# Kernel tuning notes

Measured on AMD Instinct MI355X. Metric: run time of the kernel, lower is better.

Reference implementation:

```python
import jax, jax.numpy as jnp
import numpy as np

DIM = 192
HEADS = 4
EPS = 1e-12  # F.normalize default eps


def setup_inputs() -> dict:
    key = jax.random.key(0)
    ks = jax.random.split(key, 5)
    b, c, h, w = 8, DIM, 128, 128
    x = jax.random.normal(ks[0], (b, c, h, w), dtype=jnp.float32)
    w_qkv = jax.random.normal(ks[1], (3 * DIM, DIM, 1, 1), dtype=jnp.float32) * (1.0 / np.sqrt(DIM))
    w_dw = jax.random.normal(ks[2], (3 * DIM, 1, 3, 3), dtype=jnp.float32) * (1.0 / 3.0)
    w_proj = jax.random.normal(ks[3], (DIM, DIM, 1, 1), dtype=jnp.float32) * (1.0 / np.sqrt(DIM))
    temperature = jnp.ones((HEADS, 1, 1), dtype=jnp.float32)
    return {"x": x, "w_qkv": w_qkv, "w_dw": w_dw, "w_proj": w_proj, "temperature": temperature}


def _conv1x1(x, w):
    # x: [b,c,h,w], w: [o,c,1,1] -> [b,o,h,w]
    return jnp.einsum('bchw,oc->bohw', x, w[:, :, 0, 0])


def _dwconv3x3(x, w):
    # depthwise 3x3, padding=1; x: [b,C,h,w], w: [C,1,3,3]
    C = x.shape[1]
    return jax.lax.conv_general_dilated(
        x, w, window_strides=(1, 1), padding=((1, 1), (1, 1)),
        dimension_numbers=('NCHW', 'OIHW', 'NCHW'), feature_group_count=C)


def _l2norm(x):
    n = jnp.linalg.norm(x, axis=-1, keepdims=True)
    return x / jnp.maximum(n, EPS)


def reference(x, w_qkv, w_dw, w_proj, temperature):
    b, c, h, w = x.shape
    head = HEADS
    ch = c // head  # channels per head
    qkv = _dwconv3x3(_conv1x1(x, w_qkv), w_dw)  # [b, 3c, h, w]
    q, k, v = jnp.split(qkv, 3, axis=1)  # each [b, c, h, w]

    def to_heads(t):
        # b (head ch) h w -> b head h (ch w)
        t = t.reshape(b, head, ch, h, w)
        return t.transpose(0, 1, 3, 2, 4).reshape(b, head, h, ch * w)

    q1 = _l2norm(to_heads(q))
    k1 = _l2norm(to_heads(k))
    v1 = to_heads(v)
    # attn over height dim: [b, head, h, h]
    attn = jax.nn.softmax(jnp.einsum('bhif,bhjf->bhij', q1, k1) * temperature[None], axis=-1)
    out = jnp.einsum('bhij,bhjf->bhif', attn, v1)  # [b, head, h, ch*w]
    # b head h (ch w) -> b (head ch) h w
    out = out.reshape(b, head, h, ch, w).transpose(0, 1, 3, 2, 4).reshape(b, c, h, w)
    return _conv1x1(out, w_proj)
```

## Files before the change

kernel.cpp:

```cpp
#include <hip/hip_runtime.h>
#include <hip/hip_bf16.h>

#define BB 8
#define CC 192
#define C3 576
#define NH 4
#define CH 48
#define HH 128
#define WW 128
#define HW 16384
#define FF 6144

typedef short s16x8 __attribute__((ext_vector_type(8)));
typedef float f32x4 __attribute__((ext_vector_type(4)));

constexpr size_t SPM = 32ull * 128 * 128;

constexpr size_t OFF_XT  = 0;
constexpr size_t SZ_XT   = (size_t)BB * HW * CC * 2;
constexpr size_t OFF_WQ  = OFF_XT + SZ_XT;
constexpr size_t SZ_WQ   = (size_t)C3 * CC * 2;
constexpr size_t OFF_WP  = OFF_WQ + SZ_WQ;
constexpr size_t SZ_WP   = (size_t)CC * CC * 2;
constexpr size_t OFF_RAW = OFF_WP + SZ_WP;
constexpr size_t SZ_RAW  = (size_t)BB * C3 * HW * 2;
constexpr size_t OFF_DW  = OFF_RAW + SZ_RAW;
constexpr size_t OFF_SP  = OFF_DW + SZ_RAW;
constexpr size_t OFF_ATB = OFF_SP + 8 * SPM * 4;
constexpr size_t OFF_RQ  = OFF_ATB + 32ull * 128 * 128 * 2;
constexpr size_t OFF_RK  = OFF_RQ + 32 * 128 * 4;

__device__ __forceinline__ void store_out(__hip_bfloat16* p, float v) { *p = __float2bfloat16(v); }
__device__ __forceinline__ void store_out(float* p, float v) { *p = v; }

__device__ __forceinline__ short bf16bits(float v) {
  __hip_bfloat16 t = __float2bfloat16(v);
  return *reinterpret_cast<short*>(&t);
}
__device__ __forceinline__ float b2f(short u) {
  union { unsigned int i; float f; } x;
  x.i = ((unsigned int)(unsigned short)u) << 16;
  return x.f;
}

__device__ __forceinline__ void gload16(const void* g, void* l) {
  __builtin_amdgcn_global_load_lds((const __attribute__((address_space(1))) unsigned int*)g,
                                   (__attribute__((address_space(3))) unsigned int*)l, 16, 0, 0);
}

__global__ __launch_bounds__(256) void k_cvt_t(const float* __restrict__ in,
                                               __hip_bfloat16* __restrict__ outT) {
  const int p0 = blockIdx.x * 64;
  const int c0 = blockIdx.y * 32;
  const int b = blockIdx.z;
  __shared__ float t[32][65];
  const float* ib = in + (size_t)b * CC * HW;
  const int tid = threadIdx.x;
  {
    const int c = tid >> 3, pl = (tid & 7) * 8;
    const float* s = ib + (size_t)(c0 + c) * HW + p0 + pl;
#pragma unroll
    for (int j = 0; j < 8; ++j) t[c][pl + j] = s[j];
  }
  __syncthreads();
  {
    const int pl = tid >> 2, cl = (tid & 3) * 8;
    __hip_bfloat16* d = outT + (size_t)b * HW * CC + (size_t)(p0 + pl) * CC + c0 + cl;
#pragma unroll
    for (int j = 0; j < 8; ++j) d[j] = __float2bfloat16(t[cl + j][pl]);
  }
}

__global__ __launch_bounds__(256) void k_cvt_w(const float* __restrict__ in,
                                               __hip_bfloat16* __restrict__ out, int n) {
  const int i = blockIdx.x * 256 + threadIdx.x;
  if (i < n) out[i] = __float2bfloat16(in[i]);
}

template <int M, typename OutT>
__global__ __launch_bounds__(256) void k_gemm(const __hip_bfloat16* __restrict__ xT,
                                              const __hip_bfloat16* __restrict__ Wb,
                                              OutT* __restrict__ out) {
  const int pBase = blockIdx.x * 128;
  const int mBase = blockIdx.y * 192;
  const int b = blockIdx.z;
  __shared__ __hip_bfloat16 Al[6144];
  __shared__ __hip_bfloat16 Bl[4096];
  const int tid = threadIdx.x;
  const int wave = tid >> 6, lane = tid & 63;
  const int wm = wave >> 1, wn = wave & 1;
  const __hip_bfloat16* xb = xT + (size_t)b * HW * CC;
  char* Alc = (char*)Al;
  char* Blc = (char*)Bl;
  f32x4 acc[6][4] = {};

  for (int k0 = 0; k0 < CC; k0 += 32) {
#pragma unroll
    for (int is = 0; is < 3; ++is) {
      const int ci = is * 256 + tid;
      const int row = ci & 15, kg = (ci >> 4) & 3, mf = ci >> 6;
      gload16(Wb + (size_t)(mBase + mf * 16 + row) * CC + k0 + kg * 8,
              Alc + is * 4096 + wave * 1024);
    }
#pragma unroll
    for (int is = 0; is < 2; ++is) {
      const int ci = is * 256 + tid;
      const int col = ci & 15, kg = (ci >> 4) & 3, nf = ci >> 6;
      gload16(xb + (size_t)(pBase + nf * 16 + col) * CC + k0 + kg * 8,
              Blc + is * 4096 + wave * 1024);
    }
    __syncthreads();
    s16x8 a[6], bf[4];
#pragma unroll
    for (int i = 0; i < 6; ++i) a[i] = *(const s16x8*)(Alc + ((wm * 6 + i) << 10) + (lane << 4));
#pragma unroll
    for (int j = 0; j < 4; ++j) bf[j] = *(const s16x8*)(Blc + ((wn * 4 + j) << 10) + (lane << 4));
#pragma unroll
    for (int i = 0; i < 6; ++i)
#pragma unroll
      for (int j = 0; j < 4; ++j)
        acc[i][j] = __builtin_amdgcn_mfma_f32_16x16x32_bf16(a[i], bf[j], acc[i][j], 0, 0, 0);
    __syncthreads();
  }
  OutT* ob = out + (size_t)b * M * HW;
  const int r0 = (lane >> 4) * 4, cl = lane & 15;
#pragma unroll
  for (int i = 0; i < 6; ++i) {
    const int o = mBase + (wm * 6 + i) * 16 + r0;
#pragma unroll
    for (int j = 0; j < 4; ++j) {
      const int p = pBase + (wn * 4 + j) * 16 + cl;
      OutT* dst = ob + (size_t)o * HW + p;
#pragma unroll
      for (int r = 0; r < 4; ++r) store_out(dst + (size_t)r * HW, acc[i][j][r]);
    }
  }
}

__global__ __launch_bounds__(256) void k_dwconv(const __hip_bfloat16* __restrict__ in,
                                                const float* __restrict__ wdw,
                                                __hip_bfloat16* __restrict__ out,
                                                __hip_bfloat16* __restrict__ vt) {
  const int h0 = blockIdx.x * 32;
  const int c = blockIdx.y;
  const int b = blockIdx.z;
  __shared__ __hip_bfloat16 IN[34][136];
  __shared__ char TR[8192];
  const int tid = threadIdx.x;
  const __hip_bfloat16* src = in + ((size_t)b * C3 + c) * HW;
#pragma unroll
  for (int it = 0; it < 3; ++it) {
    const int vi = it * 256 + tid;
    if (vi < 544) {
      const int r = vi >> 4, w8 = vi & 15;
      const int hg = h0 - 1 + r;
      s16x8 v = {};
      if (hg >= 0 && hg < HH) v = *(const s16x8*)(src + (size_t)hg * WW + w8 * 8);
      *(s16x8*)(&IN[r][w8 * 8]) = v;
    }
  }
  const float* wp = wdw + c * 9;
  float wgt[9];
#pragma unroll
  for (int q = 0; q < 9; ++q) wgt[q] = wp[q];
  __syncthreads();

  const int hl = tid >> 3, w0 = (tid & 7) * 16;
  float rowv[3][18];
#pragma unroll
  for (int dh = 0; dh < 3; ++dh)
#pragma unroll
    for (int e = 0; e < 18; ++e) {
      const int w = w0 - 1 + e;
      rowv[dh][e] = (w >= 0 && w < WW) ? __bfloat162float(IN[hl + dh][w]) : 0.f;
    }
  float res[16];
#pragma unroll
  for (int ww = 0; ww < 16; ++ww) {
    float acc = 0.f;
#pragma unroll
    for (int dh = 0; dh < 3; ++dh)
#pragma unroll
      for (int dwi = 0; dwi < 3; ++dwi)
        acc += rowv[dh][ww + dwi] * wgt[dh * 3 + dwi];
    res[ww] = acc;
  }
  if (c < 2 * CC) {
    short pk[16];
#pragma unroll
    for (int ww = 0; ww < 16; ++ww) pk[ww] = bf16bits(res[ww]);
    __hip_bfloat16* dst = out + ((size_t)b * C3 + c) * HW + (size_t)(h0 + hl) * WW + w0;
    *(s16x8*)dst = *(const s16x8*)pk;
    *(s16x8*)(dst + 8) = *(const s16x8*)(pk + 8);
  } else {
    const int rel = c - 2 * CC;
    const int hd = rel / CH, ch = rel - hd * CH;
#pragma unroll
    for (int ww = 0; ww < 16; ++ww) {
      const int w = w0 + ww;
      const int blk = ((w << 2) + (hl >> 3)) ^ ((w >> 3) & 3);
      *(short*)(TR + (blk << 4) + ((hl & 7) << 1)) = bf16bits(res[ww]);
    }
    __syncthreads();
    const int w = tid >> 1, half = tid & 1;
    short ot[16];
#pragma unroll
    for (int j = 0; j < 2; ++j) {
      const int hh = half * 16 + j * 8;
      const int blk = ((w << 2) + (hh >> 3)) ^ ((w >> 3) & 3);
      *(s16x8*)(ot + j * 8) = *(const s16x8*)(TR + (blk << 4));
    }
    __hip_bfloat16* vd = vt + ((size_t)(b * NH + hd) * FF + (size_t)ch * WW + w) * HH + h0 + half * 16;
    *(s16x8*)vd = *(const s16x8*)ot;
    *(s16x8*)(vd + 8) = *(const s16x8*)(ot + 8);
  }
}

__global__ __launch_bounds__(256) void k_norms(const __hip_bfloat16* __restrict__ dw,
                                               float* __restrict__ rq, float* __restrict__ rk) {
  const int i = blockIdx.x;
  const int hd = blockIdx.y;
  const int b = blockIdx.z & 7;
  const int which = blockIdx.z >> 3;
  const __hip_bfloat16* base = dw + ((size_t)b * C3 + which * CC + hd * CH) * HW + i * WW;
  float s = 0.f;
#pragma unroll
  for (int it = 0; it < 3; ++it) {
    const int idx = it * 256 + threadIdx.x;
    const int ch = idx >> 4, w8 = idx & 15;
    const s16x8 v = *(const s16x8*)(base + (size_t)ch * HW + w8 * 8);
#pragma unroll
    for (int e = 0; e < 8; ++e) {
      const float f = b2f(v[e]);
      s += f * f;
    }
  }
  __shared__ float red[4];
  const int lane = threadIdx.x & 63, wv = threadIdx.x >> 6;
#pragma unroll
  for (int off = 32; off > 0; off >>= 1) s += __shfl_down(s, off);
  if (lane == 0) red[wv] = s;
  __syncthreads();
  if (threadIdx.x == 0) {
    const float n = sqrtf(red[0] + red[1] + red[2] + red[3]);
    float* dst = which ? rk : rq;
    dst[(b * NH + hd) * HH + i] = 1.f / fmaxf(n, 1e-12f);
  }
}

__global__ __launch_bounds__(256) void k_qkm(const __hip_bfloat16* __restrict__ dw,
                                             float* __restrict__ sp) {
  const int ks = blockIdx.x;
  const int bh = blockIdx.y;
  const int b = bh >> 2, hd = bh & 3;
  const __hip_bfloat16* qb = dw + ((size_t)b * C3 + hd * CH) * HW;
  const __hip_bfloat16* kb = dw + ((size_t)b * C3 + CC + hd * CH) * HW;
  __shared__ __hip_bfloat16 Al[4096];
  __shared__ __hip_bfloat16 Bl[4096];
  char* Alc = (char*)Al;
  char* Blc = (char*)Bl;
  const int tid = threadIdx.x, wave = tid >> 6, lane = tid & 63;
  const int wm = wave >> 1, wn = wave & 1;
  f32x4 acc[4][4] = {};
  for (int chunk = 0; chunk < 24; ++chunk) {
    const int ch = ks * 6 + (chunk >> 2);
    const int w0 = (chunk & 3) * 32;
#pragma unroll
    for (int is = 0; is < 2; ++is) {
      const int ci = is * 256 + tid;
      const int row = ci & 15, kg = (ci >> 4) & 3, mf = ci >> 6;
      gload16(qb + (size_t)ch * HW + (mf * 16 + row) * WW + w0 + kg * 8,
              Alc + is * 4096 + wave * 1024);
    }
#pragma unroll
    for (int is = 0; is < 2; ++is) {
      const int ci = is * 256 + tid;
      const int col = ci & 15, kg = (ci >> 4) & 3, nf = ci >> 6;
      gload16(kb + (size_t)ch * HW + (nf * 16 + col) * WW + w0 + kg * 8,
              Blc + is * 4096 + wave * 1024);
    }
    __syncthreads();
    s16x8 a[4], bf[4];
#pragma unroll
    for (int i = 0; i < 4; ++i) a[i] = *(const s16x8*)(Alc + ((wm * 4 + i) << 10) + (lane << 4));
#pragma unroll
    for (int j = 0; j < 4; ++j) bf[j] = *(const s16x8*)(Blc + ((wn * 4 + j) << 10) + (lane << 4));
#pragma unroll
    for (int i = 0; i < 4; ++i)
#pragma unroll
      for (int j = 0; j < 4; ++j)
        acc[i][j] = __builtin_amdgcn_mfma_f32_16x16x32_bf16(a[i], bf[j], acc[i][j], 0, 0, 0);
    __syncthreads();
  }
  float* o = sp + (size_t)ks * SPM + (size_t)bh * HH * HH;
  const int r0 = (lane >> 4) * 4, cl = lane & 15;
#pragma unroll
  for (int i = 0; i < 4; ++i)
#pragma unroll
    for (int j = 0; j < 4; ++j) {
      const int ii = wm * 64 + i * 16 + r0;
      const int jj = wn * 64 + j * 16 + cl;
#pragma unroll
      for (int r = 0; r < 4; ++r) o[(ii + r) * HH + jj] = acc[i][j][r];
    }
}

__global__ __launch_bounds__(64) void k_softmax(const float* __restrict__ sp,
                                                const float* __restrict__ rq,
                                                const float* __restrict__ rk,
                                                const float* __restrict__ temp,
                                                __hip_bfloat16* __restrict__ atb) {
  const int i = blockIdx.x;
  const int bh = blockIdx.y;
  const int hd = bh & 3;
  const int lane = threadIdx.x;
  const size_t rowoff = ((size_t)bh * HH + i) * HH;
  float s0 = 0.f, s1 = 0.f;
#pragma unroll
  for (int ks = 0; ks < 8; ++ks) {
    s0 += sp[ks * SPM + rowoff + lane];
    s1 += sp[ks * SPM + rowoff + lane + 64];
  }
  const float scale = rq[bh * HH + i] * temp[hd];
  s0 *= scale * rk[bh * HH + lane];
  s1 *= scale * rk[bh * HH + lane + 64];
  float m = fmaxf(s0, s1);
#pragma unroll
  for (int off = 32; off > 0; off >>= 1) m = fmaxf(m, __shfl_xor(m, off));
  const float e0 = expf(s0 - m), e1 = expf(s1 - m);
  float ssum = e0 + e1;
#pragma unroll
  for (int off = 32; off > 0; off >>= 1) ssum += __shfl_xor(ssum, off);
  const float inv = 1.f / ssum;
  atb[rowoff + lane] = __float2bfloat16(e0 * inv);
  atb[rowoff + lane + 64] = __float2bfloat16(e1 * inv);
}

__global__ __launch_bounds__(256) void k_pvm(const __hip_bfloat16* __restrict__ atb,
                                             const __hip_bfloat16* __restrict__ vt,
                                             __hip_bfloat16* __restrict__ pvout) {
  const int fs = blockIdx.x;
  const int bh = blockIdx.y;
  const __hip_bfloat16* ab = atb + (size_t)bh * HH * HH;
  const __hip_bfloat16* vb = vt + ((size_t)bh * FF + fs * 256) * HH;
  __shared__ __hip_bfloat16 Al[4096];
  __shared__ __hip_bfloat16 Bl[8192];
  char* Alc = (char*)Al;
  char* Blc = (char*)Bl;
  const int tid = threadIdx.x, wave = tid >> 6, lane = tid & 63;
  const int wm = wave >> 1, wn = wave & 1;
  f32x4 acc[4][8] = {};
  for (int kc = 0; kc < 4; ++kc) {
    const int kj0 = kc * 32;
#pragma unroll
    for (int is = 0; is < 2; ++is) {
      const int ci = is * 256 + tid;
      const int row = ci & 15, kg = (ci >> 4) & 3, mf = ci >> 6;
      gload16(ab + (size_t)(mf * 16 + row) * HH + kj0 + kg * 8,
              Alc + is * 4096 + wave * 1024);
    }
#pragma unroll
    for (int is = 0; is < 4; ++is) {
      const int ci = is * 256 + tid;
      const int col = ci & 15, kg = (ci >> 4) & 3, nf = ci >> 6;
      gload16(vb + (size_t)(nf * 16 + col) * HH + kj0 + kg * 8,
              Blc + is * 4096 + wave * 1024);
    }
    __syncthreads();
    s16x8 a[4], bf[8];
#pragma unroll
    for (int i = 0; i < 4; ++i) a[i] = *(const s16x8*)(Alc + ((wm * 4 + i) << 10) + (lane << 4));
#pragma unroll
    for (int j = 0; j < 8; ++j) bf[j] = *(const s16x8*)(Blc + ((wn * 8 + j) << 10) + (lane << 4));
#pragma unroll
    for (int i = 0; i < 4; ++i)
#pragma unroll
      for (int j = 0; j < 8; ++j)
        acc[i][j] = __builtin_amdgcn_mfma_f32_16x16x32_bf16(a[i], bf[j], acc[i][j], 0, 0, 0);
    __syncthreads();
  }
  __hip_bfloat16* ob = pvout + (size_t)bh * HH * FF;
  const int r0 = (lane >> 4) * 4, cl = lane & 15;
#pragma unroll
  for (int i = 0; i < 4; ++i)
#pragma unroll
    for (int j = 0; j < 8; ++j) {
      const int ii = wm * 64 + i * 16 + r0;
      const int f = fs * 256 + wn * 128 + j * 16 + cl;
#pragma unroll
      for (int r = 0; r < 4; ++r) ob[(size_t)(ii + r) * FF + f] = __float2bfloat16(acc[i][j][r]);
    }
}

__global__ __launch_bounds__(256) void k_t2(const __hip_bfloat16* __restrict__ pvout,
                                            __hip_bfloat16* __restrict__ aT) {
  const int i = blockIdx.x;
  const int b = blockIdx.y;
  __shared__ char L[49152];
  const int tid = threadIdx.x;
#pragma unroll
  for (int it = 0; it < 12; ++it) {
    const int vi = it * 256 + tid;
    const int c = vi >> 4, w8 = vi & 15;
    const int hd = c / CH, ch = c - hd * CH;
    const s16x8 v = *(const s16x8*)(pvout + ((size_t)(b * NH + hd) * HH + i) * FF + ch * 128 + w8 * 8);
    const int blk = ((c << 4) + w8) ^ ((c >> 3) & 7);
    *(s16x8*)(L + (blk << 4)) = v;
  }
  __syncthreads();
#pragma unroll
  for (int it = 0; it < 12; ++it) {
    const int vi = it * 256 + tid;
    const int w = vi / 24, c8 = vi - w * 24;
    short tmp[8];
#pragma unroll
    for (int e = 0; e < 8; ++e) {
      const int c = c8 * 8 + e;
      const int blk = ((c << 4) + (w >> 3)) ^ ((c >> 3) & 7);
      tmp[e] = *(const short*)(L + (blk << 4) + ((w & 7) << 1));
    }
    *(s16x8*)(aT + ((size_t)b * HW + (size_t)i * 128 + w) * CC + c8 * 8) = *(const s16x8*)tmp;
  }
}

extern "C" void kernel_launch(void* const* d_in, const int* in_sizes, int n_in,
                              void* d_out, int out_size, void* d_ws, size_t ws_size,
                              hipStream_t stream) {
  const float* x     = (const float*)d_in[0];
  const float* wqkv  = (const float*)d_in[1];
  const float* wdw   = (const float*)d_in[2];
  const float* wproj = (const float*)d_in[3];
  const float* temp  = (const float*)d_in[4];

  char* ws = (char*)d_ws;
  __hip_bfloat16* xTb    = (__hip_bfloat16*)(ws + OFF_XT);
  __hip_bfloat16* vt     = (__hip_bfloat16*)(ws + OFF_XT);
  __hip_bfloat16* Wq     = (__hip_bfloat16*)(ws + OFF_WQ);
  __hip_bfloat16* Wp     = (__hip_bfloat16*)(ws + OFF_WP);
  __hip_bfloat16* qkvraw = (__hip_bfloat16*)(ws + OFF_RAW);
  __hip_bfloat16* pvout  = (__hip_bfloat16*)(ws + OFF_RAW);
  __hip_bfloat16* aTb    = (__hip_bfloat16*)(ws + OFF_RAW + SZ_XT);
  __hip_bfloat16* qkvdw  = (__hip_bfloat16*)(ws + OFF_DW);
  float* sp   = (float*)(ws + OFF_SP);
  __hip_bfloat16* atb = (__hip_bfloat16*)(ws + OFF_ATB);
  float* rq   = (float*)(ws + OFF_RQ);
  float* rk   = (float*)(ws + OFF_RK);

  k_cvt_w<<<dim3((C3 * CC + 255) / 256), 256, 0, stream>>>(wqkv, Wq, C3 * CC);
  k_cvt_w<<<dim3((CC * CC + 255) / 256), 256, 0, stream>>>(wproj, Wp, CC * CC);
  k_cvt_t<<<dim3(HW / 64, CC / 32, BB), 256, 0, stream>>>(x, xTb);
  k_gemm<C3, __hip_bfloat16><<<dim3(HW / 128, 3, BB), 256, 0, stream>>>(xTb, Wq, qkvraw);
  k_dwconv<<<dim3(HH / 32, C3, BB), 256, 0, stream>>>(qkvraw, wdw, qkvdw, vt);
  k_norms<<<dim3(HH, NH, 2 * BB), 256, 0, stream>>>(qkvdw, rq, rk);
  k_qkm<<<dim3(8, 32), 256, 0, stream>>>(qkvdw, sp);
  k_softmax<<<dim3(HH, 32), 64, 0, stream>>>(sp, rq, rk, temp, atb);
  k_pvm<<<dim3(24, 32), 256, 0, stream>>>(atb, vt, pvout);
  k_t2<<<dim3(HH, BB), 256, 0, stream>>>(pvout, aTb);
  k_gemm<CC, float><<<dim3(HW / 128, 1, BB), 256, 0, stream>>>(aTb, Wp, (float*)d_out);
}
```

Before: 303.4 us.

## Fuse row-norm partials into dwconv and fuse transpose into projection GEMM

The depthwise conv now computes per-row sum-of-squares partials for q and k channels and writes them to a small buffer. A lightweight 64-thread kernel reduces these partials instead of rereading the full q/k tensors. The separate transpose kernel and generic projection GEMM are replaced by one kernel that loads the PV output rows, transposes them in shared memory into MFMA fragment layout, and multiplies by the projection weights directly. The conv inner loop also uses vectorized padded LDS reads. This removes a full reread of q/k and a write/read round-trip of the transposed activations, at the cost of extra LDS traffic and a less tuned GEMM.

```diff
diff --git a/kernel.cpp b/kernel.cpp
--- a/kernel.cpp
+++ b/kernel.cpp
@@ -29,6 +29,7 @@
 constexpr size_t OFF_ATB = OFF_SP + 8 * SPM * 4;
 constexpr size_t OFF_RQ  = OFF_ATB + 32ull * 128 * 128 * 2;
 constexpr size_t OFF_RK  = OFF_RQ + 32 * 128 * 4;
+constexpr size_t OFF_PS  = OFF_SP;
 
 __device__ __forceinline__ void store_out(__hip_bfloat16* p, float v) { *p = __float2bfloat16(v); }
 __device__ __forceinline__ void store_out(float* p, float v) { *p = v; }
@@ -140,14 +141,19 @@
 __global__ __launch_bounds__(256) void k_dwconv(const __hip_bfloat16* __restrict__ in,
                                                 const float* __restrict__ wdw,
                                                 __hip_bfloat16* __restrict__ out,
-                                                __hip_bfloat16* __restrict__ vt) {
+                                                __hip_bfloat16* __restrict__ vt,
+                                                float* __restrict__ psum) {
   const int h0 = blockIdx.x * 32;
   const int c = blockIdx.y;
   const int b = blockIdx.z;
-  __shared__ __hip_bfloat16 IN[34][136];
+  __shared__ __hip_bfloat16 IN[34][152];
   __shared__ char TR[8192];
   const int tid = threadIdx.x;
   const __hip_bfloat16* src = in + ((size_t)b * C3 + c) * HW;
+  if (tid < 68) {
+    const int r = tid >> 1, col = (tid & 1) ? 136 : 0;
+    *(s16x8*)(&IN[r][col]) = (s16x8){};
+  }
 #pragma unroll
   for (int it = 0; it < 3; ++it) {
     const int vi = it * 256 + tid;
@@ -156,7 +162,7 @@
       const int hg = h0 - 1 + r;
       s16x8 v = {};
       if (hg >= 0 && hg < HH) v = *(const s16x8*)(src + (size_t)hg * WW + w8 * 8);
-      *(s16x8*)(&IN[r][w8 * 8]) = v;
+      *(s16x8*)(&IN[r][8 + w8 * 8]) = v;
     }
   }
   const float* wp = wdw + c * 9;
@@ -166,24 +172,25 @@
   __syncthreads();
 
   const int hl = tid >> 3, w0 = (tid & 7) * 16;
-  float rowv[3][18];
-#pragma unroll
-  for (int dh = 0; dh < 3; ++dh)
-#pragma unroll
-    for (int e = 0; e < 18; ++e) {
-      const int w = w0 - 1 + e;
-      rowv[dh][e] = (w >= 0 && w < WW) ? __bfloat162float(IN[hl + dh][w]) : 0.f;
-    }
-  float res[16];
-#pragma unroll
-  for (int ww = 0; ww < 16; ++ww) {
-    float acc = 0.f;
-#pragma unroll
-    for (int dh = 0; dh < 3; ++dh)
-#pragma unroll
-      for (int dwi = 0; dwi < 3; ++dwi)
-        acc += rowv[dh][ww + dwi] * wgt[dh * 3 + dwi];
-    res[ww] = acc;
+  float res[16] = {};
+#pragma unroll
+  for (int dh = 0; dh < 3; ++dh) {
+    const __hip_bfloat16* rp = &IN[hl + dh][0];
+    const s16x8 v0 = *(const s16x8*)(rp + w0);
+    const s16x8 v1 = *(const s16x8*)(rp + w0 + 8);
+    const s16x8 v2 = *(const s16x8*)(rp + w0 + 16);
+    const s16x8 v3 = *(const s16x8*)(rp + w0 + 24);
+    float rv[18];
+    rv[0] = b2f(v0[7]);
+#pragma unroll
+    for (int e = 0; e < 8; ++e) rv[1 + e] = b2f(v1[e]);
+#pragma unroll
+    for (int e = 0; e < 8; ++e) rv[9 + e] = b2f(v2[e]);
+    rv[17] = b2f(v3[0]);
+    const float wa = wgt[dh * 3], wb = wgt[dh * 3 + 1], wc = wgt[dh * 3 + 2];
+#pragma unroll
+    for (int ww = 0; ww < 16; ++ww)
+      res[ww] += rv[ww] * wa + rv[ww + 1] * wb + rv[ww + 2] * wc;
   }
   if (c < 2 * CC) {
     short pk[16];
@@ -192,6 +199,12 @@
     __hip_bfloat16* dst = out + ((size_t)b * C3 + c) * HW + (size_t)(h0 + hl) * WW + w0;
     *(s16x8*)dst = *(const s16x8*)pk;
     *(s16x8*)(dst + 8) = *(const s16x8*)(pk + 8);
+    float ss = 0.f;
+#pragma unroll
+    for (int ww = 0; ww < 16; ++ww) ss += res[ww] * res[ww];
+#pragma unroll
+    for (int off = 4; off > 0; off >>= 1) ss += __shfl_down(ss, off);
+    if ((tid & 7) == 0) psum[((size_t)b * HH + h0 + hl) * 384 + c] = ss;
   } else {
     const int rel = c - 2 * CC;
     const int hd = rel / CH, ch = rel - hd * CH;
@@ -202,47 +215,33 @@
       *(short*)(TR + (blk << 4) + ((hl & 7) << 1)) = bf16bits(res[ww]);
     }
     __syncthreads();
-    const int w = tid >> 1, half = tid & 1;
+    const int w = tid >> 1, hf = tid & 1;
     short ot[16];
 #pragma unroll
     for (int j = 0; j < 2; ++j) {
-      const int hh = half * 16 + j * 8;
+      const int hh = hf * 16 + j * 8;
       const int blk = ((w << 2) + (hh >> 3)) ^ ((w >> 3) & 3);
       *(s16x8*)(ot + j * 8) = *(const s16x8*)(TR + (blk << 4));
     }
-    __hip_bfloat16* vd = vt + ((size_t)(b * NH + hd) * FF + (size_t)ch * WW + w) * HH + h0 + half * 16;
+    __hip_bfloat16* vd = vt + ((size_t)(b * NH + hd) * FF + (size_t)ch * WW + w) * HH + h0 + hf * 16;
     *(s16x8*)vd = *(const s16x8*)ot;
     *(s16x8*)(vd + 8) = *(const s16x8*)(ot + 8);
   }
 }
 
-__global__ __launch_bounds__(256) void k_norms(const __hip_bfloat16* __restrict__ dw,
+__global__ __launch_bounds__(64) void k_norms2(const float* __restrict__ psum,
                                                float* __restrict__ rq, float* __restrict__ rk) {
   const int i = blockIdx.x;
   const int hd = blockIdx.y;
   const int b = blockIdx.z & 7;
   const int which = blockIdx.z >> 3;
-  const __hip_bfloat16* base = dw + ((size_t)b * C3 + which * CC + hd * CH) * HW + i * WW;
+  const int lane = threadIdx.x;
   float s = 0.f;
-#pragma unroll
-  for (int it = 0; it < 3; ++it) {
-    const int idx = it * 256 + threadIdx.x;
-    const int ch = idx >> 4, w8 = idx & 15;
-    const s16x8 v = *(const s16x8*)(base + (size_t)ch * HW + w8 * 8);
-#pragma unroll
-    for (int e = 0; e < 8; ++e) {
-      const float f = b2f(v[e]);
-      s += f * f;
-    }
-  }
-  __shared__ float red[4];
-  const int lane = threadIdx.x & 63, wv = threadIdx.x >> 6;
+  if (lane < 48) s = psum[((size_t)b * HH + i) * 384 + which * CC + hd * CH + lane];
 #pragma unroll
   for (int off = 32; off > 0; off >>= 1) s += __shfl_down(s, off);
-  if (lane == 0) red[wv] = s;
-  __syncthreads();
-  if (threadIdx.x == 0) {
-    const float n = sqrtf(red[0] + red[1] + red[2] + red[3]);
+  if (lane == 0) {
+    const float n = sqrtf(s);
     float* dst = which ? rk : rq;
     dst[(b * NH + hd) * HH + i] = 1.f / fmaxf(n, 1e-12f);
   }
@@ -392,34 +391,81 @@
     }
 }
 
-__global__ __launch_bounds__(256) void k_t2(const __hip_bfloat16* __restrict__ pvout,
-                                            __hip_bfloat16* __restrict__ aT) {
+__global__ __launch_bounds__(256) void k_proj(const __hip_bfloat16* __restrict__ pv,
+                                              const __hip_bfloat16* __restrict__ Wp,
+                                              float* __restrict__ out) {
   const int i = blockIdx.x;
   const int b = blockIdx.y;
-  __shared__ char L[49152];
-  const int tid = threadIdx.x;
-#pragma unroll
-  for (int it = 0; it < 12; ++it) {
-    const int vi = it * 256 + tid;
-    const int c = vi >> 4, w8 = vi & 15;
-    const int hd = c / CH, ch = c - hd * CH;
-    const s16x8 v = *(const s16x8*)(pvout + ((size_t)(b * NH + hd) * HH + i) * FF + ch * 128 + w8 * 8);
-    const int blk = ((c << 4) + w8) ^ ((c >> 3) & 7);
-    *(s16x8*)(L + (blk << 4)) = v;
-  }
-  __syncthreads();
-#pragma unroll
-  for (int it = 0; it < 12; ++it) {
-    const int vi = it * 256 + tid;
-    const int w = vi / 24, c8 = vi - w * 24;
-    short tmp[8];
-#pragma unroll
-    for (int e = 0; e < 8; ++e) {
-      const int c = c8 * 8 + e;
-      const int blk = ((c << 4) + (w >> 3)) ^ ((c >> 3) & 7);
-      tmp[e] = *(const short*)(L + (blk << 4) + ((w & 7) << 1));
-    }
-    *(s16x8*)(aT + ((size_t)b * HW + (size_t)i * 128 + w) * CC + c8 * 8) = *(const s16x8*)tmp;
+  __shared__ __hip_bfloat16 Al[6144];
+  __shared__ __hip_bfloat16 Braw[12288];
+  __shared__ __hip_bfloat16 Bfrag[12288];
+  char* Alc = (char*)Al;
+  char* Brc = (char*)Braw;
+  char* Bfc = (char*)Bfrag;
+  const int tid = threadIdx.x, wave = tid >> 6, lane = tid & 63;
+  const int wm = wave >> 1, wn = wave & 1;
+  f32x4 acc[6][4] = {};
+  for (int hf = 0; hf < 2; ++hf) {
+#pragma unroll
+    for (int it = 0; it < 6; ++it) {
+      const int vi = it * 256 + tid;
+      const int r = vi >> 4, w8 = vi & 15;
+      const int hi = (r >= 48) ? 1 : 0;
+      const int hd = hf * 2 + hi, ch = r - hi * 48;
+      const s16x8 v = *(const s16x8*)(pv + ((size_t)(b * NH + hd) * HH + i) * FF + ch * 128 + w8 * 8);
+      *(s16x8*)(Brc + r * 256 + ((w8 ^ (r & 15)) << 4)) = v;
+    }
+    __syncthreads();
+#pragma unroll
+    for (int it = 0; it < 6; ++it) {
+      const int vi = it * 256 + tid;
+      const int col = vi & 15, kg12 = (vi >> 4) % 12, nf = vi / 192;
+      const int w = nf * 16 + col;
+      short tmp[8];
+#pragma unroll
+      for (int e = 0; e < 8; ++e) {
+        const int r = kg12 * 8 + e;
+        tmp[e] = *(const short*)(Brc + r * 256 + (((w >> 3) ^ (r & 15)) << 4) + (w & 7) * 2);
+      }
+      const int kc = kg12 >> 2, kg = kg12 & 3;
+      *(s16x8*)(Bfc + (((nf * 3 + kc) * 64 + kg * 16 + col) << 4)) = *(const s16x8*)tmp;
+    }
+    for (int kc = 0; kc < 3; ++kc) {
+      const int c0 = hf * 96 + kc * 32;
+#pragma unroll
+      for (int is = 0; is < 3; ++is) {
+        const int ci = is * 256 + tid;
+        const int row = ci & 15, kg = (ci >> 4) & 3, mf = ci >> 6;
+        gload16(Wp + (size_t)(mf * 16 + row) * CC + c0 + kg * 8,
+                Alc + is * 4096 + wave * 1024);
+      }
+      __syncthreads();
+      s16x8 a[6], bf[4];
+#pragma unroll
+      for (int mi = 0; mi < 6; ++mi)
+        a[mi] = *(const s16x8*)(Alc + ((wm * 6 + mi) << 10) + (lane << 4));
+#pragma unroll
+      for (int j = 0; j < 4; ++j)
+        bf[j] = *(const s16x8*)(Bfc + ((((wn * 4 + j) * 3 + kc) * 64 + lane) << 4));
+#pragma unroll
+      for (int mi = 0; mi < 6; ++mi)
+#pragma unroll
+        for (int j = 0; j < 4; ++j)
+          acc[mi][j] = __builtin_amdgcn_mfma_f32_16x16x32_bf16(a[mi], bf[j], acc[mi][j], 0, 0, 0);
+      __syncthreads();
+    }
+  }
+  const int r0 = (lane >> 4) * 4, cl = lane & 15;
+#pragma unroll
+  for (int mi = 0; mi < 6; ++mi) {
+    const int o = (wm * 6 + mi) * 16 + r0;
+#pragma unroll
+    for (int j = 0; j < 4; ++j) {
+      const int w = (wn * 4 + j) * 16 + cl;
+      float* dst = out + ((size_t)b * CC + o) * HW + i * 128 + w;
+#pragma unroll
+      for (int r = 0; r < 4; ++r) dst[(size_t)r * HW] = acc[mi][j][r];
+    }
   }
 }
 
@@ -439,22 +485,21 @@
   __hip_bfloat16* Wp     = (__hip_bfloat16*)(ws + OFF_WP);
   __hip_bfloat16* qkvraw = (__hip_bfloat16*)(ws + OFF_RAW);
   __hip_bfloat16* pvout  = (__hip_bfloat16*)(ws + OFF_RAW);
-  __hip_bfloat16* aTb    = (__hip_bfloat16*)(ws + OFF_RAW + SZ_XT);
   __hip_bfloat16* qkvdw  = (__hip_bfloat16*)(ws + OFF_DW);
-  float* sp   = (float*)(ws + OFF_SP);
+  float* sp    = (float*)(ws + OFF_SP);
+  float* psum  = (float*)(ws + OFF_PS);
   __hip_bfloat16* atb = (__hip_bfloat16*)(ws + OFF_ATB);
-  float* rq   = (float*)(ws + OFF_RQ);
-  float* rk   = (float*)(ws + OFF_RK);
+  float* rq    = (float*)(ws + OFF_RQ);
+  float* rk    = (float*)(ws + OFF_RK);
 
   k_cvt_w<<<dim3((C3 * CC + 255) / 256), 256, 0, stream>>>(wqkv, Wq, C3 * CC);
   k_cvt_w<<<dim3((CC * CC + 255) / 256), 256, 0, stream>>>(wproj, Wp, CC * CC);
   k_cvt_t<<<dim3(HW / 64, CC / 32, BB), 256, 0, stream>>>(x, xTb);
   k_gemm<C3, __hip_bfloat16><<<dim3(HW / 128, 3, BB), 256, 0, stream>>>(xTb, Wq, qkvraw);
-  k_dwconv<<<dim3(HH / 32, C3, BB), 256, 0, stream>>>(qkvraw, wdw, qkvdw, vt);
-  k_norms<<<dim3(HH, NH, 2 * BB), 256, 0, stream>>>(qkvdw, rq, rk);
+  k_dwconv<<<dim3(HH / 32, C3, BB), 256, 0, stream>>>(qkvraw, wdw, qkvdw, vt, psum);
+  k_norms2<<<dim3(HH, NH, 2 * BB), 64, 0, stream>>>(psum, rq, rk);
   k_qkm<<<dim3(8, 32), 256, 0, stream>>>(qkvdw, sp);
   k_softmax<<<dim3(HH, 32), 64, 0, stream>>>(sp, rq, rk, temp, atb);
   k_pvm<<<dim3(24, 32), 256, 0, stream>>>(atb, vt, pvout);
-  k_t2<<<dim3(HH, BB), 256, 0, stream>>>(pvout, aTb);
-  k_gemm<CC, float><<<dim3(HW / 128, 1, BB), 256, 0, stream>>>(aTb, Wp, (float*)d_out);
-}
+  k_proj<<<dim3(HH, BB), 256, 0, stream>>>(pvout, Wp, (float*)d_out);
+}
```

After: 284.8 us. 1.07x faster.
